# Performance work log

Hardware: AMD Instinct MI355X
Metric: run time of the kernel (lower is better)

## Reference

```python
import jax, jax.numpy as jnp
import numpy as np

D_MODEL = 1024
N_HEADS = 16
HEAD_DIM = D_MODEL // N_HEADS
CHUNK = 128
B, T = 2, 2048


def setup_inputs() -> dict:
    key = jax.random.key(0)
    ks = jax.random.split(key, 5)
    x = jax.random.normal(ks[0], (B, T, D_MODEL), dtype=jnp.float32)
    mk = lambda k: jax.random.normal(k, (D_MODEL, D_MODEL), dtype=jnp.float32) * 0.02
    return {"x": x, "Wq": mk(ks[1]), "Wk": mk(ks[2]), "Wv": mk(ks[3]), "Wo": mk(ks[4])}


def _chunked_causal_attention(q, k, v, cs):
    # q,k,v: [B,H,T,D] fp32. Streaming online-softmax over kv chunks (flash-attn style).
    Bq, H, Tq, D = q.shape
    n = Tq // cs  # T divisible by chunk_size
    inv_sqrt_d = 1.0 / (D ** 0.5)
    qc = jnp.moveaxis(q.reshape(Bq, H, n, cs, D), 2, 0)  # [n,B,H,cs,D]
    kc = jnp.moveaxis(k.reshape(Bq, H, n, cs, D), 2, 0)
    vc = jnp.moveaxis(v.reshape(Bq, H, n, cs, D), 2, 0)
    ar = jnp.arange(cs)

    def per_q(qi, qb):  # qb: [B,H,cs,D]
        q_idx = qi * cs + ar

        def step(carry, kv):
            m, l, o = carry
            ki, kb, vb = kv
            s = jnp.einsum('bhqd,bhkd->bhqk', qb, kb) * inv_sqrt_d
            k_idx = ki * cs + ar
            causal = q_idx[:, None] >= k_idx[None, :]
            s = jnp.where(causal, s, -jnp.inf)
            s_max = jnp.max(s, axis=-1, keepdims=True)
            m_new = jnp.maximum(m, s_max)
            # guard fully-masked chunks (m_new = -inf)
            m_safe = jnp.where(jnp.isneginf(m_new), 0.0, m_new)
            alpha = jnp.exp(m - m_safe)
            p = jnp.exp(s - m_safe)
            o = o * alpha + jnp.einsum('bhqk,bhkd->bhqd', p, vb)
            l = l * alpha + jnp.sum(p, axis=-1, keepdims=True)
            return (m_new, l, o), None

        init = (jnp.full((Bq, H, cs, 1), -jnp.inf, dtype=jnp.float32),
                jnp.zeros((Bq, H, cs, 1), dtype=jnp.float32),
                jnp.zeros_like(qb))
        (m, l, o), _ = jax.lax.scan(step, init, (jnp.arange(n), kc, vc))
        return o / jnp.maximum(l, 1e-9)

    out = jax.vmap(per_q)(jnp.arange(n), qc)  # [n,B,H,cs,D]
    return jnp.moveaxis(out, 0, 2).reshape(Bq, H, Tq, D)


def reference(x, Wq, Wk, Wv, Wo):
    Bx, Tx, C = x.shape
    def heads(w):
        return (x @ w.T).reshape(Bx, Tx, N_HEADS, HEAD_DIM).transpose(0, 2, 1, 3)
    q, k, v = heads(Wq), heads(Wk), heads(Wv)
    y = _chunked_causal_attention(q, k, v, CHUNK)  # [B,H,T,D]
    y = y.transpose(0, 2, 1, 3).reshape(Bx, Tx, C)
    return y @ Wo.T
```

## Files before the change

kernel.cpp:

```cpp
#include <hip/hip_runtime.h>
#include <hip/hip_bf16.h>
#include <stdint.h>

typedef __bf16 bf16;
typedef __bf16 bf16x8 __attribute__((ext_vector_type(8)));
typedef __bf16 bf16x4 __attribute__((ext_vector_type(4)));
typedef float  f32x4  __attribute__((ext_vector_type(4)));

#define DM 1024
#define NH 16
#define HD 64
#define TT 2048

#define QSCALE 0.18033688011112042f

__global__ void cvt_all(const float* __restrict__ x,  const float* __restrict__ wq,
                        const float* __restrict__ wk, const float* __restrict__ wv,
                        const float* __restrict__ wo,
                        bf16* __restrict__ xb,  bf16* __restrict__ wqb,
                        bf16* __restrict__ wkb, bf16* __restrict__ wvb,
                        bf16* __restrict__ wob) {
  const int i = (blockIdx.x * blockDim.x + threadIdx.x) * 4;
  const float* src; bf16* dst; int off;
  if (i < 4194304)      { src = x;  dst = xb;  off = i; }
  else {
    const int j = i - 4194304;
    const int w = j >> 20;
    off = j & 1048575;
    src = (w == 0) ? wq : (w == 1) ? wk : (w == 2) ? wv : wo;
    dst = (w == 0) ? wqb : (w == 1) ? wkb : (w == 2) ? wvb : wob;
  }
  const float4 v = *reinterpret_cast<const float4*>(src + off);
  bf16x4 o = { (bf16)v.x, (bf16)v.y, (bf16)v.z, (bf16)v.w };
  *reinterpret_cast<bf16x4*>(dst + off) = o;
}

static __device__ __forceinline__ void gload_lds16(const bf16* g, bf16* l) {
  __builtin_amdgcn_global_load_lds(
      (__attribute__((address_space(1))) void*)g,
      (__attribute__((address_space(3))) void*)l, 16, 0, 0);
}

static __device__ __forceinline__ int swzb(int lin) {
  return lin ^ (((lin >> 7) & 7) << 4);
}

__launch_bounds__(256, 3)
__global__ void gemm_qkv(const bf16* __restrict__ X, const bf16* __restrict__ Wq,
                         const bf16* __restrict__ Wk, const bf16* __restrict__ Wv,
                         bf16* __restrict__ Qb, bf16* __restrict__ Kb,
                         bf16* __restrict__ Vtb) {
  __shared__ bf16 As[128 * 32];
  __shared__ bf16 Bs[128 * 32];
  const int tid  = threadIdx.x;
  const int lane = tid & 63;
  const int wv   = tid >> 6;
  const int lg   = lane >> 4, lc = lane & 15;
  const int m0   = blockIdx.x * 128;
  const int ng   = blockIdx.y * 128;
  const int which = ng >> 10;
  const bf16* W = (which == 0) ? Wq : ((which == 1) ? Wk : Wv);
  const int n0 = ng & 1023;
  const int wm = wv >> 1, wn = wv & 1;

  f32x4 acc[4][4] = {};

  for (int k0 = 0; k0 < DM; k0 += 32) {
#pragma unroll
    for (int c = 0; c < 2; ++c) {
      const int e   = wv * 512 + c * 2048 + lane * 8;
      const int row = e >> 5, col = e & 31;
      gload_lds16(X + (size_t)(m0 + row) * DM + k0 + col, &As[wv * 512 + c * 2048]);
      gload_lds16(W + (size_t)(n0 + row) * DM + k0 + col, &Bs[wv * 512 + c * 2048]);
    }
    __syncthreads();
    bf16x8 a[4], b[4];
#pragma unroll
    for (int i = 0; i < 4; ++i)
      a[i] = *reinterpret_cast<const bf16x8*>(&As[(wm * 64 + i * 16 + lc) * 32 + lg * 8]);
#pragma unroll
    for (int j = 0; j < 4; ++j)
      b[j] = *reinterpret_cast<const bf16x8*>(&Bs[(wn * 64 + j * 16 + lc) * 32 + lg * 8]);
#pragma unroll
    for (int i = 0; i < 4; ++i)
#pragma unroll
      for (int j = 0; j < 4; ++j)
        acc[i][j] = __builtin_amdgcn_mfma_f32_16x16x32_bf16(a[i], b[j], acc[i][j], 0, 0, 0);
    __syncthreads();
  }

#pragma unroll
  for (int i = 0; i < 4; ++i) {
    const int mg = m0 + wm * 64 + i * 16 + lg * 4;
    const int bb = mg >> 11, t = mg & 2047;
#pragma unroll
    for (int j = 0; j < 4; ++j) {
      const int nl = n0 + wn * 64 + j * 16 + lc;
      const int h = nl >> 6, d = nl & 63;
      const int bh = bb * NH + h;
      const f32x4 v = acc[i][j];
      if (which == 0) {
        bf16* p = Qb + ((size_t)bh * TT + t) * HD + d;
#pragma unroll
        for (int r = 0; r < 4; ++r) p[r * HD] = (bf16)(v[r] * QSCALE);
      } else if (which == 1) {
        bf16* p = Kb + ((size_t)bh * TT + t) * HD + d;
#pragma unroll
        for (int r = 0; r < 4; ++r) p[r * HD] = (bf16)v[r];
      } else {
        bf16x4 pk = { (bf16)v[0], (bf16)v[1], (bf16)v[2], (bf16)v[3] };
        *reinterpret_cast<bf16x4*>(Vtb + ((size_t)bh * HD + d) * TT + t) = pk;
      }
    }
  }
}

#define KPAD 72

__launch_bounds__(256, 2)
__global__ void attn_fwd(const bf16* __restrict__ Qb, const bf16* __restrict__ Kb,
                         const bf16* __restrict__ Vtb, bf16* __restrict__ Yb) {
  __shared__ bf16 Ks[2][4096];
  __shared__ bf16 Vs[2][4096];
  __shared__ bf16 Ps[4][16 * KPAD];

  const int tid  = threadIdx.x;
  const int lane = tid & 63;
  const int wv   = tid >> 6;
  const int lg   = lane >> 4;
  const int lc   = lane & 15;
  const int bh   = blockIdx.x & 31;
  const int pr   = blockIdx.x >> 5;
  const int qblkA = 16 + pr, qblkB = 15 - pr;
  const int nt0  = qblkA + 1;
  const int NT   = 33;

  const bf16* Qg = Qb  + (size_t)bh * TT * HD;
  const bf16* Kg = Kb  + (size_t)bh * TT * HD;
  const bf16* Vg = Vtb + (size_t)bh * HD * TT;

  bf16x8 qA0, qA1, qB0, qB1;
  qA0 = *reinterpret_cast<const bf16x8*>(Qg + (size_t)(qblkA * 64 + wv * 16 + lc) * HD + 0  + lg * 8);
  qA1 = *reinterpret_cast<const bf16x8*>(Qg + (size_t)(qblkA * 64 + wv * 16 + lc) * HD + 32 + lg * 8);
  qB0 = *reinterpret_cast<const bf16x8*>(Qg + (size_t)(qblkB * 64 + wv * 16 + lc) * HD + 0  + lg * 8);
  qB1 = *reinterpret_cast<const bf16x8*>(Qg + (size_t)(qblkB * 64 + wv * 16 + lc) * HD + 32 + lg * 8);

  int dstb[2], koff[2], voff[2];
#pragma unroll
  for (int c = 0; c < 2; ++c) {
    const int base = (wv * 2 + c) * 1024;
    const int lin  = base + lane * 16;
    dstb[c] = base;
    koff[c] = swzb(lin);
    voff[c] = (lin >> 7) * (TT * 2) + (swzb(lin) & 127);
  }

  auto STAGE = [&](int b, int kv) {
#pragma unroll
    for (int c = 0; c < 2; ++c) {
      gload_lds16((const bf16*)((const char*)Kg + (size_t)kv * 8192 + koff[c]),
                  (bf16*)((char*)Ks[b] + dstb[c]));
      gload_lds16((const bf16*)((const char*)Vg + (size_t)kv * 128 + voff[c]),
                  (bf16*)((char*)Vs[b] + dstb[c]));
    }
  };

  f32x4 o[4] = {};
  float m_run = -INFINITY, l_run = 0.f;
  int   q0 = qblkA * 64;
  bf16x8 qf0 = qA0, qf1 = qA1;
  bf16* Pw = Ps[wv];
  const int b_ = bh >> 4, h_ = bh & 15;

  STAGE(0, 0);

  int cur = 0;
  for (int ti = 0; ti < NT; ++ti) {
    const int kv = (ti < nt0) ? ti : ti - nt0;
    const int k0 = kv * 64;

    if (ti + 1 < NT) {
      const int tn = ti + 1;
      STAGE(cur ^ 1, (tn < nt0) ? tn : tn - nt0);
      asm volatile("s_waitcnt vmcnt(4)" ::: "memory");
    } else {
      asm volatile("s_waitcnt vmcnt(0)" ::: "memory");
    }
    __builtin_amdgcn_s_barrier();
    __builtin_amdgcn_sched_barrier(0);

    const char* ksb = (const char*)Ks[cur];
    const char* vsb = (const char*)Vs[cur];

    f32x4 s[4] = {};
    __builtin_amdgcn_s_setprio(1);
#pragma unroll
    for (int kvf = 0; kvf < 4; ++kvf) {
      const bf16x8 k0f = *reinterpret_cast<const bf16x8*>(
          ksb + swzb((kvf * 16 + lc) * 128 + lg * 16));
      s[kvf] = __builtin_amdgcn_mfma_f32_16x16x32_bf16(k0f, qf0, s[kvf], 0, 0, 0);
      const bf16x8 k1f = *reinterpret_cast<const bf16x8*>(
          ksb + swzb((kvf * 16 + lc) * 128 + 64 + lg * 16));
      s[kvf] = __builtin_amdgcn_mfma_f32_16x16x32_bf16(k1f, qf1, s[kvf], 0, 0, 0);
    }
    __builtin_amdgcn_s_setprio(0);

    const int qw = q0 + wv * 16;
    if (k0 + 63 > qw) {
      const int q = qw + lc;
#pragma unroll
      for (int kvf = 0; kvf < 4; ++kvf)
#pragma unroll
        for (int r = 0; r < 4; ++r)
          if (k0 + kvf * 16 + lg * 4 + r > q) s[kvf][r] = -INFINITY;
    }

    float t0 = fmaxf(fmaxf(s[0][0], s[0][1]), fmaxf(s[0][2], s[0][3]));
    float t1 = fmaxf(fmaxf(s[1][0], s[1][1]), fmaxf(s[1][2], s[1][3]));
    float t2 = fmaxf(fmaxf(s[2][0], s[2][1]), fmaxf(s[2][2], s[2][3]));
    float t3 = fmaxf(fmaxf(s[3][0], s[3][1]), fmaxf(s[3][2], s[3][3]));
    float rmax = fmaxf(fmaxf(t0, t1), fmaxf(t2, t3));
    rmax = fmaxf(rmax, __shfl_xor(rmax, 16));
    rmax = fmaxf(rmax, __shfl_xor(rmax, 32));

    const float mn = fmaxf(m_run, rmax);
    const float alpha = __builtin_amdgcn_exp2f(m_run - mn);
    m_run = mn;

#pragma unroll
    for (int kvf = 0; kvf < 4; ++kvf)
#pragma unroll
      for (int r = 0; r < 4; ++r)
        s[kvf][r] = __builtin_amdgcn_exp2f(s[kvf][r] - mn);

    float u0 = (s[0][0] + s[0][1]) + (s[0][2] + s[0][3]);
    float u1 = (s[1][0] + s[1][1]) + (s[1][2] + s[1][3]);
    float u2 = (s[2][0] + s[2][1]) + (s[2][2] + s[2][3]);
    float u3 = (s[3][0] + s[3][1]) + (s[3][2] + s[3][3]);
    float rsum = (u0 + u1) + (u2 + u3);
    rsum += __shfl_xor(rsum, 16);
    rsum += __shfl_xor(rsum, 32);
    l_run = l_run * alpha + rsum;

#pragma unroll
    for (int df = 0; df < 4; ++df)
#pragma unroll
      for (int r = 0; r < 4; ++r) o[df][r] *= alpha;

#pragma unroll
    for (int kvf = 0; kvf < 4; ++kvf) {
      bf16x4 pk = { (bf16)s[kvf][0], (bf16)s[kvf][1],
                    (bf16)s[kvf][2], (bf16)s[kvf][3] };
      *reinterpret_cast<bf16x4*>(&Pw[lc * KPAD + kvf * 16 + lg * 4]) = pk;
    }

    __builtin_amdgcn_s_setprio(1);
#pragma unroll
    for (int ks = 0; ks < 2; ++ks) {
      const bf16x8 pf = *reinterpret_cast<const bf16x8*>(
          &Pw[lc * KPAD + ks * 32 + lg * 8]);
#pragma unroll
      for (int df = 0; df < 4; ++df) {
        const bf16x8 vf = *reinterpret_cast<const bf16x8*>(
            vsb + swzb((df * 16 + lc) * 128 + ks * 64 + lg * 16));
        o[df] = __builtin_amdgcn_mfma_f32_16x16x32_bf16(vf, pf, o[df], 0, 0, 0);
      }
    }
    __builtin_amdgcn_s_setprio(0);

    if (ti == nt0 - 1) {
      const float linv = 1.f / fmaxf(l_run, 1e-9f);
      const int q = q0 + wv * 16 + lc;
#pragma unroll
      for (int df = 0; df < 4; ++df) {
        bf16x4 yv = { (bf16)(o[df][0] * linv), (bf16)(o[df][1] * linv),
                      (bf16)(o[df][2] * linv), (bf16)(o[df][3] * linv) };
        *reinterpret_cast<bf16x4*>(
            Yb + ((size_t)(b_ * TT + q)) * DM + h_ * HD + df * 16 + lg * 4) = yv;
        o[df] = f32x4{};
      }
      m_run = -INFINITY; l_run = 0.f;
      q0 = qblkB * 64;
      qf0 = qB0; qf1 = qB1;
    }

    __builtin_amdgcn_s_barrier();
    cur ^= 1;
  }

  {
    const float linv = 1.f / fmaxf(l_run, 1e-9f);
    const int q = q0 + wv * 16 + lc;
#pragma unroll
    for (int df = 0; df < 4; ++df) {
      bf16x4 yv = { (bf16)(o[df][0] * linv), (bf16)(o[df][1] * linv),
                    (bf16)(o[df][2] * linv), (bf16)(o[df][3] * linv) };
      *reinterpret_cast<bf16x4*>(
          Yb + ((size_t)(b_ * TT + q)) * DM + h_ * HD + df * 16 + lg * 4) = yv;
    }
  }
}

__launch_bounds__(256, 2)
__global__ void gemm_out(const bf16* __restrict__ Y, const bf16* __restrict__ Wo,
                         float* __restrict__ Out) {
  __shared__ bf16 As[64 * 32];
  __shared__ bf16 Bs[128 * 32];
  const int tid  = threadIdx.x;
  const int lane = tid & 63;
  const int wv   = tid >> 6;
  const int lg   = lane >> 4, lc = lane & 15;
  const int m0   = blockIdx.x * 64;
  const int n0   = blockIdx.y * 128;
  const int wm = wv >> 1, wn = wv & 1;

  f32x4 acc[2][4] = {};

  for (int k0 = 0; k0 < DM; k0 += 32) {
    {
      const int e   = wv * 512 + lane * 8;
      const int row = e >> 5, col = e & 31;
      gload_lds16(Y + (size_t)(m0 + row) * DM + k0 + col, &As[wv * 512]);
    }
#pragma unroll
    for (int c = 0; c < 2; ++c) {
      const int e   = wv * 1024 + c * 512 + lane * 8;
      const int row = e >> 5, col = e & 31;
      gload_lds16(Wo + (size_t)(n0 + row) * DM + k0 + col, &Bs[wv * 1024 + c * 512]);
    }
    __syncthreads();
    bf16x8 a[2], b[4];
#pragma unroll
    for (int i = 0; i < 2; ++i)
      a[i] = *reinterpret_cast<const bf16x8*>(&As[(wm * 32 + i * 16 + lc) * 32 + lg * 8]);
#pragma unroll
    for (int j = 0; j < 4; ++j)
      b[j] = *reinterpret_cast<const bf16x8*>(&Bs[(wn * 64 + j * 16 + lc) * 32 + lg * 8]);
#pragma unroll
    for (int i = 0; i < 2; ++i)
#pragma unroll
      for (int j = 0; j < 4; ++j)
        acc[i][j] = __builtin_amdgcn_mfma_f32_16x16x32_bf16(a[i], b[j], acc[i][j], 0, 0, 0);
    __syncthreads();
  }

#pragma unroll
  for (int i = 0; i < 2; ++i) {
    const int mg = m0 + wm * 32 + i * 16 + lg * 4;
#pragma unroll
    for (int j = 0; j < 4; ++j) {
      const int n = n0 + wn * 64 + j * 16 + lc;
#pragma unroll
      for (int r = 0; r < 4; ++r)
        Out[(size_t)(mg + r) * DM + n] = acc[i][j][r];
    }
  }
}

extern "C" void kernel_launch(void* const* d_in, const int* in_sizes, int n_in,
                              void* d_out, int out_size, void* d_ws, size_t ws_size,
                              hipStream_t stream) {
  const float* x  = (const float*)d_in[0];
  const float* Wq = (const float*)d_in[1];
  const float* Wk = (const float*)d_in[2];
  const float* Wv = (const float*)d_in[3];
  const float* Wo = (const float*)d_in[4];
  float* out = (float*)d_out;
  char* ws = (char*)d_ws;
  const size_t MB = 1024 * 1024;

  bf16* xb  = (bf16*)(ws + 0);
  bf16* wqb = (bf16*)(ws + 8  * MB);
  bf16* wkb = (bf16*)(ws + 10 * MB);
  bf16* wvb = (bf16*)(ws + 12 * MB);
  bf16* wob = (bf16*)(ws + 14 * MB);
  bf16* Qb  = (bf16*)(ws + 16 * MB);
  bf16* Kb  = (bf16*)(ws + 24 * MB);
  bf16* Vtb = (bf16*)(ws + 32 * MB);
  bf16* yb  = xb;

  cvt_all<<<8192, 256, 0, stream>>>(x, Wq, Wk, Wv, Wo, xb, wqb, wkb, wvb, wob);
  gemm_qkv<<<dim3(32, 24), 256, 0, stream>>>(xb, wqb, wkb, wvb, Qb, Kb, Vtb);
  attn_fwd<<<512, 256, 0, stream>>>(Qb, Kb, Vtb, yb);
  gemm_out<<<dim3(64, 8), 256, 0, stream>>>(yb, wob, out);
}
```

Before: 110.7 us.

## Split paired causal q-blocks into one q-block per workgroup, longest first

Each attention workgroup previously handled two q-blocks (a long and a short one paired for balance, 33 kv tiles total). Now each workgroup handles a single q-block, launched in descending order of work, so the grid doubles to 1024 blocks. Occupancy is raised to 3 blocks per SIMD and the PV MFMA is moved ahead of the row-sum reduction to overlap. This trades more per-block prologue overhead and less intra-block balance for more parallelism and a simpler loop.

```diff
diff --git a/kernel.cpp b/kernel.cpp
--- a/kernel.cpp
+++ b/kernel.cpp
@@ -117,7 +117,7 @@
 
 #define KPAD 72
 
-__launch_bounds__(256, 2)
+__launch_bounds__(256, 3)
 __global__ void attn_fwd(const bf16* __restrict__ Qb, const bf16* __restrict__ Kb,
                          const bf16* __restrict__ Vtb, bf16* __restrict__ Yb) {
   __shared__ bf16 Ks[2][4096];
@@ -130,20 +130,18 @@
   const int lg   = lane >> 4;
   const int lc   = lane & 15;
   const int bh   = blockIdx.x & 31;
-  const int pr   = blockIdx.x >> 5;
-  const int qblkA = 16 + pr, qblkB = 15 - pr;
-  const int nt0  = qblkA + 1;
-  const int NT   = 33;
+  const int qblk = 31 - (blockIdx.x >> 5);
+  const int q0   = qblk * 64;
+  const int NT   = qblk + 1;
 
   const bf16* Qg = Qb  + (size_t)bh * TT * HD;
   const bf16* Kg = Kb  + (size_t)bh * TT * HD;
   const bf16* Vg = Vtb + (size_t)bh * HD * TT;
 
-  bf16x8 qA0, qA1, qB0, qB1;
-  qA0 = *reinterpret_cast<const bf16x8*>(Qg + (size_t)(qblkA * 64 + wv * 16 + lc) * HD + 0  + lg * 8);
-  qA1 = *reinterpret_cast<const bf16x8*>(Qg + (size_t)(qblkA * 64 + wv * 16 + lc) * HD + 32 + lg * 8);
-  qB0 = *reinterpret_cast<const bf16x8*>(Qg + (size_t)(qblkB * 64 + wv * 16 + lc) * HD + 0  + lg * 8);
-  qB1 = *reinterpret_cast<const bf16x8*>(Qg + (size_t)(qblkB * 64 + wv * 16 + lc) * HD + 32 + lg * 8);
+  const bf16x8 qf0 = *reinterpret_cast<const bf16x8*>(
+      Qg + (size_t)(q0 + wv * 16 + lc) * HD + 0  + lg * 8);
+  const bf16x8 qf1 = *reinterpret_cast<const bf16x8*>(
+      Qg + (size_t)(q0 + wv * 16 + lc) * HD + 32 + lg * 8);
 
   int dstb[2], koff[2], voff[2];
 #pragma unroll
@@ -167,21 +165,18 @@
 
   f32x4 o[4] = {};
   float m_run = -INFINITY, l_run = 0.f;
-  int   q0 = qblkA * 64;
-  bf16x8 qf0 = qA0, qf1 = qA1;
   bf16* Pw = Ps[wv];
   const int b_ = bh >> 4, h_ = bh & 15;
+  const int qw = q0 + wv * 16;
 
   STAGE(0, 0);
 
   int cur = 0;
   for (int ti = 0; ti < NT; ++ti) {
-    const int kv = (ti < nt0) ? ti : ti - nt0;
-    const int k0 = kv * 64;
+    const int k0 = ti * 64;
 
     if (ti + 1 < NT) {
-      const int tn = ti + 1;
-      STAGE(cur ^ 1, (tn < nt0) ? tn : tn - nt0);
+      STAGE(cur ^ 1, ti + 1);
       asm volatile("s_waitcnt vmcnt(4)" ::: "memory");
     } else {
       asm volatile("s_waitcnt vmcnt(0)" ::: "memory");
@@ -205,7 +200,6 @@
     }
     __builtin_amdgcn_s_setprio(0);
 
-    const int qw = q0 + wv * 16;
     if (k0 + 63 > qw) {
       const int q = qw + lc;
 #pragma unroll
@@ -232,6 +226,32 @@
 #pragma unroll
       for (int r = 0; r < 4; ++r)
         s[kvf][r] = __builtin_amdgcn_exp2f(s[kvf][r] - mn);
+
+#pragma unroll
+    for (int df = 0; df < 4; ++df)
+#pragma unroll
+      for (int r = 0; r < 4; ++r) o[df][r] *= alpha;
+
+#pragma unroll
+    for (int kvf = 0; kvf < 4; ++kvf) {
+      bf16x4 pk = { (bf16)s[kvf][0], (bf16)s[kvf][1],
+                    (bf16)s[kvf][2], (bf16)s[kvf][3] };
+      *reinterpret_cast<bf16x4*>(&Pw[lc * KPAD + kvf * 16 + lg * 4]) = pk;
+    }
+
+    __builtin_amdgcn_s_setprio(1);
+#pragma unroll
+    for (int ks = 0; ks < 2; ++ks) {
+      const bf16x8 pf = *reinterpret_cast<const bf16x8*>(
+          &Pw[lc * KPAD + ks * 32 + lg * 8]);
+#pragma unroll
+      for (int df = 0; df < 4; ++df) {
+        const bf16x8 vf = *reinterpret_cast<const bf16x8*>(
+            vsb + swzb((df * 16 + lc) * 128 + ks * 64 + lg * 16));
+        o[df] = __builtin_amdgcn_mfma_f32_16x16x32_bf16(vf, pf, o[df], 0, 0, 0);
+      }
+    }
+    __builtin_amdgcn_s_setprio(0);
 
     float u0 = (s[0][0] + s[0][1]) + (s[0][2] + s[0][3]);
     float u1 = (s[1][0] + s[1][1]) + (s[1][2] + s[1][3]);
@@ -242,55 +262,13 @@
     rsum += __shfl_xor(rsum, 32);
     l_run = l_run * alpha + rsum;
 
-#pragma unroll
-    for (int df = 0; df < 4; ++df)
-#pragma unroll
-      for (int r = 0; r < 4; ++r) o[df][r] *= alpha;
-
-#pragma unroll
-    for (int kvf = 0; kvf < 4; ++kvf) {
-      bf16x4 pk = { (bf16)s[kvf][0], (bf16)s[kvf][1],
-                    (bf16)s[kvf][2], (bf16)s[kvf][3] };
-      *reinterpret_cast<bf16x4*>(&Pw[lc * KPAD + kvf * 16 + lg * 4]) = pk;
-    }
-
-    __builtin_amdgcn_s_setprio(1);
-#pragma unroll
-    for (int ks = 0; ks < 2; ++ks) {
-      const bf16x8 pf = *reinterpret_cast<const bf16x8*>(
-          &Pw[lc * KPAD + ks * 32 + lg * 8]);
-#pragma unroll
-      for (int df = 0; df < 4; ++df) {
-        const bf16x8 vf = *reinterpret_cast<const bf16x8*>(
-            vsb + swzb((df * 16 + lc) * 128 + ks * 64 + lg * 16));
-        o[df] = __builtin_amdgcn_mfma_f32_16x16x32_bf16(vf, pf, o[df], 0, 0, 0);
-      }
-    }
-    __builtin_amdgcn_s_setprio(0);
-
-    if (ti == nt0 - 1) {
-      const float linv = 1.f / fmaxf(l_run, 1e-9f);
-      const int q = q0 + wv * 16 + lc;
-#pragma unroll
-      for (int df = 0; df < 4; ++df) {
-        bf16x4 yv = { (bf16)(o[df][0] * linv), (bf16)(o[df][1] * linv),
-                      (bf16)(o[df][2] * linv), (bf16)(o[df][3] * linv) };
-        *reinterpret_cast<bf16x4*>(
-            Yb + ((size_t)(b_ * TT + q)) * DM + h_ * HD + df * 16 + lg * 4) = yv;
-        o[df] = f32x4{};
-      }
-      m_run = -INFINITY; l_run = 0.f;
-      q0 = qblkB * 64;
-      qf0 = qB0; qf1 = qB1;
-    }
-
     __builtin_amdgcn_s_barrier();
     cur ^= 1;
   }
 
   {
     const float linv = 1.f / fmaxf(l_run, 1e-9f);
-    const int q = q0 + wv * 16 + lc;
+    const int q = qw + lc;
 #pragma unroll
     for (int df = 0; df < 4; ++df) {
       bf16x4 yv = { (bf16)(o[df][0] * linv), (bf16)(o[df][1] * linv),
@@ -381,6 +359,6 @@
 
   cvt_all<<<8192, 256, 0, stream>>>(x, Wq, Wk, Wv, Wo, xb, wqb, wkb, wvb, wob);
   gemm_qkv<<<dim3(32, 24), 256, 0, stream>>>(xb, wqb, wkb, wvb, Qb, Kb, Vtb);
-  attn_fwd<<<512, 256, 0, stream>>>(Qb, Kb, Vtb, yb);
+  attn_fwd<<<1024, 256, 0, stream>>>(Qb, Kb, Vtb, yb);
   gemm_out<<<dim3(64, 8), 256, 0, stream>>>(yb, wob, out);
 }
```

New measurement: 107.7 us. 1.03x faster.
